# Optimization experiments

Hardware: AMD Instinct MI355X
Metric: run time of the kernel (lower is better)

Reference implementation:

```python
import jax, jax.numpy as jnp
import numpy as np

B, T, C = 256, 2048, 39   # batch, time, nb_filters
NB = 8                     # number of dilation levels (2**0 .. 2**7)
K = 2                      # kernel size
NC = 8                     # num_classes
EPS = 1e-5                 # BatchNorm eps (eval mode)


def _causal_conv(x, w, b, d):
    """x: [B,C,T], w: [Cout,Cin,K], left-pad (K-1)*d for causality."""
    k = w.shape[-1]
    y = jax.lax.conv_general_dilated(
        x, w, window_strides=(1,), padding=[((k - 1) * d, 0)],
        rhs_dilation=(d,), dimension_numbers=('NCH', 'OIH', 'NCH'))
    return y + b[None, :, None]


def _bn(x, g, be, m, v):
    # eval-mode BatchNorm1d with running stats
    return g[None, :, None] * (x - m[None, :, None]) * jax.lax.rsqrt(v + EPS)[None, :, None] + be[None, :, None]


def _block(x, w, b, g, be, m, v, d):
    # Temporal_Aware_Block, eval mode (dropout = identity).
    # w: [2,C,C,K], b/g/be/m/v: [2,C]
    y = jax.nn.relu(_bn(_causal_conv(x, w[0], b[0], d), g[0], be[0], m[0], v[0]))
    y = jax.nn.relu(_bn(_causal_conv(y, w[1], b[1], d), g[1], be[1], m[1], v[1]))
    # causal conv preserves length, so the 1x1 residual conv branch is never taken
    return x * jax.nn.sigmoid(y)


def setup_inputs() -> dict:
    key = jax.random.key(0)
    ks = jax.random.split(key, 24)
    f = lambda k, s: jax.random.normal(k, s, dtype=jnp.float32) * 0.1
    return {
        'inputs': jax.random.normal(ks[0], (B, T, C), dtype=jnp.float32),
        'conv1x1_w': f(ks[1], (C, C, 1)),
        'conv1x1_b': f(ks[2], (C,)),
        'fw_conv_w': f(ks[3], (NB, 2, C, C, K)),
        'fw_conv_b': f(ks[4], (NB, 2, C)),
        'fw_gamma': 1.0 + f(ks[5], (NB, 2, C)),
        'fw_beta': f(ks[6], (NB, 2, C)),
        'fw_mean': f(ks[7], (NB, 2, C)),
        'fw_var': jax.random.uniform(ks[8], (NB, 2, C), dtype=jnp.float32, minval=0.5, maxval=1.5),
        'bw_conv_w': f(ks[9], (NB, 2, C, C, K)),
        'bw_conv_b': f(ks[10], (NB, 2, C)),
        'bw_gamma': 1.0 + f(ks[11], (NB, 2, C)),
        'bw_beta': f(ks[12], (NB, 2, C)),
        'bw_mean': f(ks[13], (NB, 2, C)),
        'bw_var': jax.random.uniform(ks[14], (NB, 2, C), dtype=jnp.float32, minval=0.5, maxval=1.5),
        'wl_kernel': f(ks[15], (NB, 1)),
        'cls_w': f(ks[16], (NC, C)),
        'cls_b': f(ks[17], (NC,)),
    }


def reference(inputs, conv1x1_w, conv1x1_b,
              fw_conv_w, fw_conv_b, fw_gamma, fw_beta, fw_mean, fw_var,
              bw_conv_w, bw_conv_b, bw_gamma, bw_beta, bw_mean, bw_var,
              wl_kernel, cls_w, cls_b):
    x = jnp.transpose(inputs, (0, 2, 1))           # [B,C,T]
    fwd = _causal_conv(x, conv1x1_w, conv1x1_b, 1)
    bwd = _causal_conv(x[:, :, ::-1], conv1x1_w, conv1x1_b, 1)
    skips = []
    for i in range(NB):
        d = 2 ** i
        fwd = _block(fwd, fw_conv_w[i], fw_conv_b[i], fw_gamma[i], fw_beta[i], fw_mean[i], fw_var[i], d)
        bwd = _block(bwd, bw_conv_w[i], bw_conv_b[i], bw_gamma[i], bw_beta[i], bw_mean[i], bw_var[i], d)
        skips.append(jnp.mean(fwd + bwd, axis=-1))  # [B,C]
    g = jnp.stack(skips, axis=-1)                   # [B,C,NB]
    x2 = jnp.einsum('bcn,no->bc', g, wl_kernel)     # WeightLayer matmul + squeeze
    logits = x2 @ cls_w.T + cls_b                   # [B,NC]
    return jax.nn.log_softmax(logits, axis=1)
```

## Files before the change

### kernel.cpp

```cpp
#include <hip/hip_runtime.h>
#include <math.h>

#define BATCH 256
#define TT    2048
#define CC    39
#define CP    40
#define NBLK  8
#define KK    2
#define NCLS  8
#define BN_EPS 1e-5f

typedef __attribute__((ext_vector_type(8))) short short8;
typedef __attribute__((ext_vector_type(4))) float floatx4;

__device__ __forceinline__ unsigned short f2b(float f) {
    union { float f; unsigned u; } v; v.f = f;
    unsigned r = v.u + 0x7FFF + ((v.u >> 16) & 1);
    return (unsigned short)(r >> 16);
}
__device__ __forceinline__ unsigned cvtpk(float lo, float hi) {
    unsigned r;
    asm("v_cvt_pk_bf16_f32 %0, %1, %2" : "=v"(r) : "v"(lo), "v"(hi));
    return r;
}
__device__ __forceinline__ float blo(unsigned u) {
    union { unsigned v; float f; } k; k.v = u << 16; return k.f;
}
__device__ __forceinline__ float bhi(unsigned u) {
    union { unsigned v; float f; } k; k.v = u & 0xffff0000u; return k.f;
}

#define WFB_PER   (2*3*3*512)
#define WFB_TOTAL (2*NBLK*WFB_PER)
#define BFB_TOTAL (2*NBLK*2*48)
#define WFF_TOTAL (3*2*512)
#define BFF_TOTAL 48

__global__ void fold_kernel(const float* __restrict__ fw_w, const float* __restrict__ fw_b,
                            const float* __restrict__ fw_g, const float* __restrict__ fw_be,
                            const float* __restrict__ fw_m, const float* __restrict__ fw_v,
                            const float* __restrict__ bw_w, const float* __restrict__ bw_b,
                            const float* __restrict__ bw_g, const float* __restrict__ bw_be,
                            const float* __restrict__ bw_m, const float* __restrict__ bw_v,
                            const float* __restrict__ c1w, const float* __restrict__ c1b,
                            unsigned short* __restrict__ wfb, float* __restrict__ bfb,
                            unsigned short* __restrict__ wff, float* __restrict__ bff) {
    int idx = blockIdx.x * blockDim.x + threadIdx.x;
    if (idx < WFB_TOTAL) {
        int i = idx;
        int reg = i & 7;   i >>= 3;
        int lane = i & 63; i >>= 6;
        int sl = i % 3;    i /= 3;
        int ct = i % 3;    i /= 3;
        int layer = i & 1; i >>= 1;
        int blk = i & 7;   i >>= 3;
        int dir = i;
        int co = ct * 16 + (lane & 15);
        int kin = ((lane >> 4) << 3) + reg;
        int p = kin >> 4;
        int ci = sl * 16 + (kin & 15);
        float val = 0.f;
        if (co < CC && ci < CC) {
            const float* w = dir ? bw_w : fw_w;
            const float* g = dir ? bw_g : fw_g;
            const float* v = dir ? bw_v : fw_v;
            int il = blk * 2 + layer;
            float sc = g[il * CC + co] * rsqrtf(v[il * CC + co] + BN_EPS);
            val = w[((size_t)(il * CC + co) * CC + ci) * KK + p] * sc;
        }
        wfb[idx] = f2b(val);
        return;
    }
    idx -= WFB_TOTAL;
    if (idx < BFB_TOTAL) {
        int co = idx % 48;
        int i = idx / 48;
        int layer = i & 1; i >>= 1;
        int blk = i & 7;   i >>= 3;
        int dir = i;
        float val = 0.f;
        if (co < CC) {
            const float* b  = dir ? bw_b  : fw_b;
            const float* g  = dir ? bw_g  : fw_g;
            const float* be = dir ? bw_be : fw_be;
            const float* m  = dir ? bw_m  : fw_m;
            const float* v  = dir ? bw_v  : fw_v;
            int r = (blk * 2 + layer) * CC + co;
            float sc = g[r] * rsqrtf(v[r] + BN_EPS);
            val = (b[r] - m[r]) * sc + be[r];
        }
        bfb[idx] = val;
        return;
    }
    idx -= BFB_TOTAL;
    if (idx < WFF_TOTAL) {
        int i = idx;
        int reg = i & 7;   i >>= 3;
        int lane = i & 63; i >>= 6;
        int sl = i & 1;    i >>= 1;
        int ct = i;
        int co = ct * 16 + (lane & 15);
        int ci = sl * 32 + ((lane >> 4) << 3) + reg;
        float val = (co < CC && ci < CC) ? c1w[co * CC + ci] : 0.f;
        wff[idx] = f2b(val);
        return;
    }
    idx -= WFF_TOTAL;
    if (idx < BFF_TOTAL) {
        bff[idx] = (idx < CC) ? c1b[idx] : 0.f;
    }
}

__global__ __launch_bounds__(256) void front_mfma(const float* __restrict__ in,
                                                  const unsigned short* __restrict__ wf,
                                                  const float* __restrict__ bias,
                                                  unsigned short* __restrict__ out) {
    __shared__ unsigned short xt[256 * CP + 32];
    const int dir = blockIdx.z, b = blockIdx.y, t0 = blockIdx.x * 256;
    const int tid = threadIdx.x, lane = tid & 63, wave = tid >> 6;
    const int c = lane & 15, g = lane >> 4;
    const int stmin = dir ? (TT - t0 - 256) : t0;
    const float* src = in + ((size_t)b * TT + stmin) * CC;

    unsigned* xd = (unsigned*)xt;
    for (int e = tid; e < 256 * 20; e += 256) {
        int row = e / 20, cp = e - row * 20;
        int c0 = cp * 2;
        float f0 = src[(size_t)row * CC + c0];
        float f1 = (c0 + 1 < CC) ? src[(size_t)row * CC + c0 + 1] : 0.f;
        xd[row * 20 + cp] = cvtpk(f0, f1);
    }
    if (tid < 16) ((unsigned*)(xt + 256 * CP))[tid] = 0;
    __syncthreads();

    short8 Wf[3][2];
#pragma unroll
    for (int ct = 0; ct < 3; ++ct)
#pragma unroll
        for (int sl = 0; sl < 2; ++sl)
            Wf[ct][sl] = *(const short8*)(wf + (((ct * 2 + sl) * 64 + lane) << 3));
    float bs[3][4];
#pragma unroll
    for (int ct = 0; ct < 3; ++ct)
#pragma unroll
        for (int j = 0; j < 4; ++j) bs[ct][j] = bias[ct * 16 + g * 4 + j];

    for (int mt = wave; mt < 16; mt += 4) {
        int row = (mt << 4) + c;
        const unsigned short* bp = xt + row * CP;
        floatx4 acc[3];
#pragma unroll
        for (int ct = 0; ct < 3; ++ct)
            acc[ct] = floatx4{bs[ct][0], bs[ct][1], bs[ct][2], bs[ct][3]};
#pragma unroll
        for (int sl = 0; sl < 2; ++sl) {
            short8 B = *(const short8*)(bp + sl * 32 + g * 8);
#pragma unroll
            for (int ct = 0; ct < 3; ++ct)
                acc[ct] = __builtin_amdgcn_mfma_f32_16x16x32_bf16(Wf[ct][sl], B, acc[ct], 0, 0, 0);
        }
        int t = dir ? (t0 + 255 - row) : (t0 + row);
        unsigned short* op = out + ((size_t)(dir * BATCH + b) * TT + t) * CP;
#pragma unroll
        for (int ct = 0; ct < 3; ++ct) {
            if (ct == 2 && g >= 2) continue;
            uint2 v;
            v.x = cvtpk(acc[ct][0], acc[ct][1]);
            v.y = cvtpk(acc[ct][2], acc[ct][3]);
            *(uint2*)(op + ct * 16 + g * 4) = v;
        }
    }
}

__global__ __launch_bounds__(256) void block_mfma(const unsigned short* __restrict__ xg,
                                                  unsigned short* __restrict__ yg,
                                                  const unsigned short* __restrict__ wf_all,
                                                  const float* __restrict__ bf_all,
                                                  float* __restrict__ skipPart,
                                                  int d, int blk, int Tt, int writeOut) {
    extern __shared__ char ldsraw[];
    const int dir = blockIdx.z, b = blockIdx.y, tile = blockIdx.x;
    const int t0 = tile * Tt;
    const int tid = threadIdx.x, lane = tid & 63, wave = tid >> 6;
    const int c = lane & 15, g = lane >> 4;
    const int tapoff = (g >> 1) ? d : 0;
    const int koff8 = (g & 1) << 3;
    const int rows_x = Tt + 2 * d;
    const int M1 = (Tt + d + 15) >> 4;
    const int rows_y1 = M1 << 4;
    const int rows_real = Tt + d;

    unsigned short* xt = (unsigned short*)ldsraw;
    unsigned short* y1 = xt + rows_x * CP + 32;
    float* stash = (float*)(y1 + rows_y1 * CP + 32);

    const size_t cbase = (size_t)(dir * BATCH + b) * TT * CP;
    const unsigned short* wf = wf_all + (size_t)(dir * NBLK + blk) * WFB_PER;
    const float* bf = bf_all + (size_t)(dir * NBLK + blk) * 96;

    {
        const uint4* gsrc = (const uint4*)(xg + cbase);
        uint4* ldst = (uint4*)xt;
        int base_t = t0 - 2 * d;
        int nch = rows_x * 5;
        for (int ch = tid; ch < nch; ch += 256) {
            int row = ch / 5;
            int t = base_t + row;
            uint4 v;
            if (t < 0) { v.x = v.y = v.z = v.w = 0u; }
            else       { v = gsrc[(size_t)t * 5 + (ch - row * 5)]; }
            ldst[ch] = v;
        }
        if (tid < 16) ((unsigned*)(xt + (size_t)rows_x * CP))[tid] = 0;
        else if (tid < 32) ((unsigned*)(y1 + (size_t)rows_y1 * CP))[tid - 16] = 0;
    }
    __syncthreads();

    short8 Wf[3][3];
#pragma unroll
    for (int ct = 0; ct < 3; ++ct)
#pragma unroll
        for (int sl = 0; sl < 3; ++sl)
            Wf[ct][sl] = *(const short8*)(wf + ((((0 * 3 + ct) * 3 + sl) * 64 + lane) << 3));
    float bs[3][4];
#pragma unroll
    for (int ct = 0; ct < 3; ++ct)
#pragma unroll
        for (int j = 0; j < 4; ++j) bs[ct][j] = bf[ct * 16 + g * 4 + j];

    for (int mt = wave; mt < M1; mt += 4) {
        int j0 = mt << 4;
        int brow = j0 + c + tapoff;
        const unsigned short* bp = xt + brow * CP + koff8;
        floatx4 acc[3];
#pragma unroll
        for (int ct = 0; ct < 3; ++ct)
            acc[ct] = floatx4{bs[ct][0], bs[ct][1], bs[ct][2], bs[ct][3]};
#pragma unroll
        for (int sl = 0; sl < 3; ++sl) {
            short8 B = *(const short8*)(bp + sl * 16);
#pragma unroll
            for (int ct = 0; ct < 3; ++ct)
                acc[ct] = __builtin_amdgcn_mfma_f32_16x16x32_bf16(Wf[ct][sl], B, acc[ct], 0, 0, 0);
        }
        int r = j0 + c;
        bool dead = (t0 - d + r < 0) || (r >= rows_real);
        unsigned short* yp = y1 + r * CP;
#pragma unroll
        for (int ct = 0; ct < 3; ++ct) {
            if (ct == 2 && g >= 2) continue;
            uint2 v;
            v.x = cvtpk(fmaxf(acc[ct][0], 0.f), fmaxf(acc[ct][1], 0.f));
            v.y = cvtpk(fmaxf(acc[ct][2], 0.f), fmaxf(acc[ct][3], 0.f));
            if (dead) { v.x = 0u; v.y = 0u; }
            *(uint2*)(yp + ct * 16 + g * 4) = v;
        }
    }
    __syncthreads();

#pragma unroll
    for (int ct = 0; ct < 3; ++ct)
#pragma unroll
        for (int sl = 0; sl < 3; ++sl)
            Wf[ct][sl] = *(const short8*)(wf + ((((1 * 3 + ct) * 3 + sl) * 64 + lane) << 3));
#pragma unroll
    for (int ct = 0; ct < 3; ++ct)
#pragma unroll
        for (int j = 0; j < 4; ++j) bs[ct][j] = bf[48 + ct * 16 + g * 4 + j];

    float sums[3][4];
#pragma unroll
    for (int ct = 0; ct < 3; ++ct)
#pragma unroll
        for (int j = 0; j < 4; ++j) sums[ct][j] = 0.f;

    const int M2w = Tt >> 6;
    for (int mi = 0; mi < M2w; ++mi) {
        int j0 = (wave * M2w + mi) << 4;
        int brow = j0 + c + tapoff;
        const unsigned short* bp = y1 + brow * CP + koff8;
        floatx4 acc[3];
#pragma unroll
        for (int ct = 0; ct < 3; ++ct)
            acc[ct] = floatx4{bs[ct][0], bs[ct][1], bs[ct][2], bs[ct][3]};
#pragma unroll
        for (int sl = 0; sl < 3; ++sl) {
            short8 B = *(const short8*)(bp + sl * 16);
#pragma unroll
            for (int ct = 0; ct < 3; ++ct)
                acc[ct] = __builtin_amdgcn_mfma_f32_16x16x32_bf16(Wf[ct][sl], B, acc[ct], 0, 0, 0);
        }
        int r = j0 + c;
        const unsigned short* xrow = xt + (r + 2 * d) * CP;
        unsigned short* orow = yg + cbase + (size_t)(t0 + r) * CP;
#pragma unroll
        for (int ct = 0; ct < 3; ++ct) {
            uint2 xv = *(const uint2*)(xrow + ct * 16 + g * 4);
            float g0 = blo(xv.x) * __builtin_amdgcn_rcpf(1.f + __expf(-acc[ct][0]));
            float g1 = bhi(xv.x) * __builtin_amdgcn_rcpf(1.f + __expf(-acc[ct][1]));
            float g2 = blo(xv.y) * __builtin_amdgcn_rcpf(1.f + __expf(-acc[ct][2]));
            float g3 = bhi(xv.y) * __builtin_amdgcn_rcpf(1.f + __expf(-acc[ct][3]));
            sums[ct][0] += g0; sums[ct][1] += g1;
            sums[ct][2] += g2; sums[ct][3] += g3;
            if (writeOut && !(ct == 2 && g >= 2)) {
                uint2 v;
                v.x = cvtpk(g0, g1);
                v.y = cvtpk(g2, g3);
                *(uint2*)(orow + ct * 16 + g * 4) = v;
            }
        }
    }
#pragma unroll
    for (int ct = 0; ct < 3; ++ct)
#pragma unroll
        for (int j = 0; j < 4; ++j) {
            float v = sums[ct][j];
            v += __shfl_xor(v, 1, 64);
            v += __shfl_xor(v, 2, 64);
            v += __shfl_xor(v, 4, 64);
            v += __shfl_xor(v, 8, 64);
            sums[ct][j] = v;
        }
    if (c == 0) {
#pragma unroll
        for (int ct = 0; ct < 3; ++ct)
#pragma unroll
            for (int j = 0; j < 4; ++j)
                stash[wave * 48 + ct * 16 + g * 4 + j] = sums[ct][j];
    }
    __syncthreads();
    if (tid < CC) {
        float s = stash[tid] + stash[48 + tid] + stash[96 + tid] + stash[144 + tid];
        skipPart[(((size_t)(blk * 2 + dir) * BATCH + b) * CC + tid) * 16 + tile] = s;
    }
}

__global__ __launch_bounds__(64) void tail_kernel(const float* __restrict__ skipPart,
                                                  const float* __restrict__ wl,
                                                  const float* __restrict__ cw,
                                                  const float* __restrict__ cb,
                                                  float* __restrict__ out) {
    __shared__ float xs[CC];
    int b = blockIdx.x;
    int cth = threadIdx.x;
    if (cth < CC) {
        float x2 = 0.f;
        for (int i = 0; i < NBLK; ++i) {
            float wli = wl[i] * (1.0f / TT);
            int nt = (i == NBLK - 1) ? 16 : 8;
            for (int dirn = 0; dirn < 2; ++dirn) {
                const float* sp = skipPart + (((size_t)(i * 2 + dirn) * BATCH + b) * CC + cth) * 16;
                float s = 0.f;
                for (int tl = 0; tl < nt; ++tl) s += sp[tl];
                x2 = fmaf(s, wli, x2);
            }
        }
        xs[cth] = x2;
    }
    __syncthreads();
    if (threadIdx.x == 0) {
        float lg[NCLS];
        float mx = -1e30f;
        for (int o = 0; o < NCLS; ++o) {
            float a = cb[o];
#pragma unroll
            for (int cc2 = 0; cc2 < CC; ++cc2) a = fmaf(cw[o * CC + cc2], xs[cc2], a);
            lg[o] = a;
            mx = fmaxf(mx, a);
        }
        float se = 0.f;
        for (int o = 0; o < NCLS; ++o) se += expf(lg[o] - mx);
        float lse = logf(se) + mx;
        for (int o = 0; o < NCLS; ++o) out[b * NCLS + o] = lg[o] - lse;
    }
}

extern "C" void kernel_launch(void* const* d_in, const int* in_sizes, int n_in,
                              void* d_out, int out_size, void* d_ws, size_t ws_size,
                              hipStream_t stream) {
    const float* inputs = (const float*)d_in[0];
    const float* c1w    = (const float*)d_in[1];
    const float* c1b    = (const float*)d_in[2];
    const float* fw_w   = (const float*)d_in[3];
    const float* fw_b   = (const float*)d_in[4];
    const float* fw_g   = (const float*)d_in[5];
    const float* fw_be  = (const float*)d_in[6];
    const float* fw_m   = (const float*)d_in[7];
    const float* fw_v   = (const float*)d_in[8];
    const float* bw_w   = (const float*)d_in[9];
    const float* bw_b   = (const float*)d_in[10];
    const float* bw_g   = (const float*)d_in[11];
    const float* bw_be  = (const float*)d_in[12];
    const float* bw_m   = (const float*)d_in[13];
    const float* bw_v   = (const float*)d_in[14];
    const float* wl     = (const float*)d_in[15];
    const float* clsw   = (const float*)d_in[16];
    const float* clsb   = (const float*)d_in[17];

    const size_t bufsz = (size_t)2 * BATCH * TT * CP;
    unsigned short* buf0 = (unsigned short*)d_ws;
    unsigned short* buf1 = buf0 + bufsz;
    float* skip = (float*)(buf1 + bufsz);
    const size_t skipsz = (size_t)NBLK * 2 * BATCH * CC * 16;
    unsigned short* wfb = (unsigned short*)(skip + skipsz);
    float* bfb = (float*)(wfb + WFB_TOTAL);
    unsigned short* wff = (unsigned short*)(bfb + BFB_TOTAL);
    float* bff = (float*)(wff + WFF_TOTAL);

    {
        int tot = WFB_TOTAL + BFB_TOTAL + WFF_TOTAL + BFF_TOTAL;
        fold_kernel<<<(tot + 255) / 256, 256, 0, stream>>>(
            fw_w, fw_b, fw_g, fw_be, fw_m, fw_v,
            bw_w, bw_b, bw_g, bw_be, bw_m, bw_v, c1w, c1b,
            wfb, bfb, wff, bff);
    }

    front_mfma<<<dim3(TT / 256, BATCH, 2), 256, 0, stream>>>(inputs, wff, bff, buf0);

    unsigned short* cur = buf0;
    unsigned short* nxt = buf1;
    for (int i = 0; i < NBLK; ++i) {
        int d = 1 << i;
        int Tt = (d == 128) ? 128 : 256;
        int ntl = TT / Tt;
        int rows_x = Tt + 2 * d;
        int M1 = (Tt + d + 15) >> 4;
        int rows_y1 = M1 << 4;
        size_t lds = ((size_t)(rows_x * CP + 32) + (size_t)(rows_y1 * CP + 32)) * 2 + 4 * 48 * 4;
        block_mfma<<<dim3(ntl, BATCH, 2), 256, lds, stream>>>(
            cur, nxt, wfb, bfb, skip, d, i, Tt, (i < NBLK - 1) ? 1 : 0);
        unsigned short* tmp = cur; cur = nxt; nxt = tmp;
    }

    tail_kernel<<<BATCH, 64, 0, stream>>>(skip, wl, clsw, clsb, (float*)d_out);
}
```

Measured before the change: 543.3 us.

## Use direct global-to-LDS loads, template block kernel on dilation, repack K-slices

Tile loading into LDS now uses the global_load_lds builtin, with out-of-range rows served from a zeroed pad buffer, so data no longer passes through VGPRs. The block kernel is templated on dilation and tile length, making loop bounds and offsets compile-time constants. The weight layout for the third K-slice is repacked so that both conv taps of channels 32-39 share one MFMA, which removes a wasted padded slice. The y1 LDS row stride changes to 44 to reduce bank conflicts. This adds a memset, an extra workspace region and eight template instantiations, and the repacked weight layout and loader must match exactly for results to stay correct.

```diff
diff --git a/kernel.cpp b/kernel.cpp
--- a/kernel.cpp
+++ b/kernel.cpp
@@ -5,6 +5,7 @@
 #define TT    2048
 #define CC    39
 #define CP    40
+#define Y1ST  44
 #define NBLK  8
 #define KK    2
 #define NCLS  8
@@ -28,6 +29,11 @@
 }
 __device__ __forceinline__ float bhi(unsigned u) {
     union { unsigned v; float f; } k; k.v = u & 0xffff0000u; return k.f;
+}
+__device__ __forceinline__ void gl_lds16(const void* g, void* l) {
+    __builtin_amdgcn_global_load_lds(
+        (const __attribute__((address_space(1))) unsigned int*)g,
+        (__attribute__((address_space(3))) unsigned int*)l, 16, 0, 0);
 }
 
 #define WFB_PER   (2*3*3*512)
@@ -35,6 +41,7 @@
 #define BFB_TOTAL (2*NBLK*2*48)
 #define WFF_TOTAL (3*2*512)
 #define BFF_TOTAL 48
+#define ZPAD_SHORTS (256 * CP)
 
 __global__ void fold_kernel(const float* __restrict__ fw_w, const float* __restrict__ fw_b,
                             const float* __restrict__ fw_g, const float* __restrict__ fw_be,
@@ -55,17 +62,25 @@
         int layer = i & 1; i >>= 1;
         int blk = i & 7;   i >>= 3;
         int dir = i;
+        int g = lane >> 4;
         int co = ct * 16 + (lane & 15);
-        int kin = ((lane >> 4) << 3) + reg;
-        int p = kin >> 4;
-        int ci = sl * 16 + (kin & 15);
+        int p, ci; bool ok = true;
+        if (sl < 2) {
+            int kin = (g << 3) + reg;
+            p = kin >> 4;
+            ci = sl * 16 + (kin & 15);
+        } else {
+            p = g & 1;
+            ci = 32 + reg;
+            ok = (g < 2);
+        }
         float val = 0.f;
-        if (co < CC && ci < CC) {
+        if (ok && co < CC && ci < CC) {
             const float* w = dir ? bw_w : fw_w;
-            const float* g = dir ? bw_g : fw_g;
-            const float* v = dir ? bw_v : fw_v;
+            const float* gam = dir ? bw_g : fw_g;
+            const float* var = dir ? bw_v : fw_v;
             int il = blk * 2 + layer;
-            float sc = g[il * CC + co] * rsqrtf(v[il * CC + co] + BN_EPS);
+            float sc = gam[il * CC + co] * rsqrtf(var[il * CC + co] + BN_EPS);
             val = w[((size_t)(il * CC + co) * CC + ci) * KK + p] * sc;
         }
         wfb[idx] = f2b(val);
@@ -172,49 +187,53 @@
     }
 }
 
+template <int D, int TtC>
 __global__ __launch_bounds__(256) void block_mfma(const unsigned short* __restrict__ xg,
                                                   unsigned short* __restrict__ yg,
                                                   const unsigned short* __restrict__ wf_all,
                                                   const float* __restrict__ bf_all,
                                                   float* __restrict__ skipPart,
-                                                  int d, int blk, int Tt, int writeOut) {
+                                                  const unsigned short* __restrict__ zpad,
+                                                  int blk, int writeOut) {
+    constexpr int ROWS_X   = TtC + 2 * D;
+    constexpr int NCH      = ROWS_X * 5;
+    constexpr int NIT      = (NCH + 255) / 256;
+    constexpr int XT_SHORTS = NIT * 256 * 8;
+    constexpr int M1       = (TtC + D + 15) / 16;
+    constexpr int ROWS_Y1  = M1 * 16;
+    constexpr int ROWS_REAL = TtC + D;
+    constexpr int Y1_SHORTS = ROWS_Y1 * Y1ST + 8;
+    constexpr int M2W      = TtC / 64;
+
     extern __shared__ char ldsraw[];
+    unsigned short* xt = (unsigned short*)ldsraw;
+    unsigned short* y1 = xt + XT_SHORTS;
+    float* stash = (float*)(y1 + Y1_SHORTS);
+
     const int dir = blockIdx.z, b = blockIdx.y, tile = blockIdx.x;
-    const int t0 = tile * Tt;
+    const int t0 = tile * TtC;
     const int tid = threadIdx.x, lane = tid & 63, wave = tid >> 6;
     const int c = lane & 15, g = lane >> 4;
-    const int tapoff = (g >> 1) ? d : 0;
-    const int koff8 = (g & 1) << 3;
-    const int rows_x = Tt + 2 * d;
-    const int M1 = (Tt + d + 15) >> 4;
-    const int rows_y1 = M1 << 4;
-    const int rows_real = Tt + d;
-
-    unsigned short* xt = (unsigned short*)ldsraw;
-    unsigned short* y1 = xt + rows_x * CP + 32;
-    float* stash = (float*)(y1 + rows_y1 * CP + 32);
 
     const size_t cbase = (size_t)(dir * BATCH + b) * TT * CP;
     const unsigned short* wf = wf_all + (size_t)(dir * NBLK + blk) * WFB_PER;
     const float* bf = bf_all + (size_t)(dir * NBLK + blk) * 96;
 
     {
-        const uint4* gsrc = (const uint4*)(xg + cbase);
-        uint4* ldst = (uint4*)xt;
-        int base_t = t0 - 2 * d;
-        int nch = rows_x * 5;
-        for (int ch = tid; ch < nch; ch += 256) {
-            int row = ch / 5;
-            int t = base_t + row;
-            uint4 v;
-            if (t < 0) { v.x = v.y = v.z = v.w = 0u; }
-            else       { v = gsrc[(size_t)t * 5 + (ch - row * 5)]; }
-            ldst[ch] = v;
-        }
-        if (tid < 16) ((unsigned*)(xt + (size_t)rows_x * CP))[tid] = 0;
-        else if (tid < 32) ((unsigned*)(y1 + (size_t)rows_y1 * CP))[tid - 16] = 0;
-    }
-    __syncthreads();
+        const unsigned short* gx = xg + cbase;
+#pragma unroll
+        for (int it = 0; it < NIT; ++it) {
+            int chunk = it * 256 + wave * 64 + lane;
+            unsigned row = (unsigned)chunk / 5u;
+            int sub = chunk - (int)row * 5;
+            int t = t0 - 2 * D + (int)row;
+            const unsigned short* src = (chunk < NCH && t >= 0)
+                ? (gx + (size_t)t * CP + sub * 8)
+                : (zpad + ((row & 255u) * CP + sub * 8));
+            unsigned short* dst = xt + (size_t)(it * 256 + wave * 64) * 8;
+            gl_lds16(src, dst);
+        }
+    }
 
     short8 Wf[3][3];
 #pragma unroll
@@ -228,24 +247,30 @@
 #pragma unroll
         for (int j = 0; j < 4; ++j) bs[ct][j] = bf[ct * 16 + g * 4 + j];
 
+    __syncthreads();
+
+    const int r01off = (g >> 1) * D;
+    const int r2off  = (g & 1) * D;
+    const int koff8  = (g & 1) << 3;
+
     for (int mt = wave; mt < M1; mt += 4) {
         int j0 = mt << 4;
-        int brow = j0 + c + tapoff;
-        const unsigned short* bp = xt + brow * CP + koff8;
+        const unsigned short* bp01 = xt + (j0 + c + r01off) * CP + koff8;
+        const unsigned short* bp2  = xt + (j0 + c + r2off) * CP + 32;
+        short8 B0 = *(const short8*)(bp01);
+        short8 B1 = *(const short8*)(bp01 + 16);
+        short8 B2 = *(const short8*)(bp2);
         floatx4 acc[3];
 #pragma unroll
-        for (int ct = 0; ct < 3; ++ct)
+        for (int ct = 0; ct < 3; ++ct) {
             acc[ct] = floatx4{bs[ct][0], bs[ct][1], bs[ct][2], bs[ct][3]};
-#pragma unroll
-        for (int sl = 0; sl < 3; ++sl) {
-            short8 B = *(const short8*)(bp + sl * 16);
-#pragma unroll
-            for (int ct = 0; ct < 3; ++ct)
-                acc[ct] = __builtin_amdgcn_mfma_f32_16x16x32_bf16(Wf[ct][sl], B, acc[ct], 0, 0, 0);
+            acc[ct] = __builtin_amdgcn_mfma_f32_16x16x32_bf16(Wf[ct][0], B0, acc[ct], 0, 0, 0);
+            acc[ct] = __builtin_amdgcn_mfma_f32_16x16x32_bf16(Wf[ct][1], B1, acc[ct], 0, 0, 0);
+            acc[ct] = __builtin_amdgcn_mfma_f32_16x16x32_bf16(Wf[ct][2], B2, acc[ct], 0, 0, 0);
         }
         int r = j0 + c;
-        bool dead = (t0 - d + r < 0) || (r >= rows_real);
-        unsigned short* yp = y1 + r * CP;
+        bool dead = (t0 - D + r < 0) || (r >= ROWS_REAL);
+        unsigned short* yp = y1 + r * Y1ST;
 #pragma unroll
         for (int ct = 0; ct < 3; ++ct) {
             if (ct == 2 && g >= 2) continue;
@@ -274,24 +299,24 @@
 #pragma unroll
         for (int j = 0; j < 4; ++j) sums[ct][j] = 0.f;
 
-    const int M2w = Tt >> 6;
-    for (int mi = 0; mi < M2w; ++mi) {
-        int j0 = (wave * M2w + mi) << 4;
-        int brow = j0 + c + tapoff;
-        const unsigned short* bp = y1 + brow * CP + koff8;
+#pragma unroll
+    for (int mi = 0; mi < M2W; ++mi) {
+        int j0 = (wave * M2W + mi) << 4;
+        const unsigned short* bp01 = y1 + (j0 + c + r01off) * Y1ST + koff8;
+        const unsigned short* bp2  = y1 + (j0 + c + r2off) * Y1ST + 32;
+        short8 B0 = *(const short8*)(bp01);
+        short8 B1 = *(const short8*)(bp01 + 16);
+        short8 B2 = *(const short8*)(bp2);
         floatx4 acc[3];
 #pragma unroll
-        for (int ct = 0; ct < 3; ++ct)
+        for (int ct = 0; ct < 3; ++ct) {
             acc[ct] = floatx4{bs[ct][0], bs[ct][1], bs[ct][2], bs[ct][3]};
-#pragma unroll
-        for (int sl = 0; sl < 3; ++sl) {
-            short8 B = *(const short8*)(bp + sl * 16);
-#pragma unroll
-            for (int ct = 0; ct < 3; ++ct)
-                acc[ct] = __builtin_amdgcn_mfma_f32_16x16x32_bf16(Wf[ct][sl], B, acc[ct], 0, 0, 0);
+            acc[ct] = __builtin_amdgcn_mfma_f32_16x16x32_bf16(Wf[ct][0], B0, acc[ct], 0, 0, 0);
+            acc[ct] = __builtin_amdgcn_mfma_f32_16x16x32_bf16(Wf[ct][1], B1, acc[ct], 0, 0, 0);
+            acc[ct] = __builtin_amdgcn_mfma_f32_16x16x32_bf16(Wf[ct][2], B2, acc[ct], 0, 0, 0);
         }
         int r = j0 + c;
-        const unsigned short* xrow = xt + (r + 2 * d) * CP;
+        const unsigned short* xrow = xt + (r + 2 * D) * CP;
         unsigned short* orow = yg + cbase + (size_t)(t0 + r) * CP;
 #pragma unroll
         for (int ct = 0; ct < 3; ++ct) {
@@ -333,6 +358,16 @@
         float s = stash[tid] + stash[48 + tid] + stash[96 + tid] + stash[144 + tid];
         skipPart[(((size_t)(blk * 2 + dir) * BATCH + b) * CC + tid) * 16 + tile] = s;
     }
+}
+
+static inline size_t lds_bytes_for(int D, int Tt) {
+    int rows_x = Tt + 2 * D;
+    int nch = rows_x * 5;
+    int nit = (nch + 255) / 256;
+    int xt_shorts = nit * 256 * 8;
+    int m1 = (Tt + D + 15) / 16;
+    int y1_shorts = m1 * 16 * Y1ST + 8;
+    return (size_t)(xt_shorts + y1_shorts) * 2 + 192 * 4;
 }
 
 __global__ __launch_bounds__(64) void tail_kernel(const float* __restrict__ skipPart,
@@ -406,6 +441,9 @@
     float* bfb = (float*)(wfb + WFB_TOTAL);
     unsigned short* wff = (unsigned short*)(bfb + BFB_TOTAL);
     float* bff = (float*)(wff + WFF_TOTAL);
+    unsigned short* zpad = (unsigned short*)(bff + BFF_TOTAL);
+
+    hipMemsetAsync(zpad, 0, ZPAD_SHORTS * sizeof(unsigned short), stream);
 
     {
         int tot = WFB_TOTAL + BFB_TOTAL + WFF_TOTAL + BFF_TOTAL;
@@ -419,18 +457,24 @@
 
     unsigned short* cur = buf0;
     unsigned short* nxt = buf1;
+#define LAUNCH_BLOCK(DD, TTC)                                                        \
+    block_mfma<DD, TTC><<<dim3(TT / TTC, BATCH, 2), 256, lds_bytes_for(DD, TTC),     \
+                          stream>>>(cur, nxt, wfb, bfb, skip, zpad, i,               \
+                                    (i < NBLK - 1) ? 1 : 0)
     for (int i = 0; i < NBLK; ++i) {
-        int d = 1 << i;
-        int Tt = (d == 128) ? 128 : 256;
-        int ntl = TT / Tt;
-        int rows_x = Tt + 2 * d;
-        int M1 = (Tt + d + 15) >> 4;
-        int rows_y1 = M1 << 4;
-        size_t lds = ((size_t)(rows_x * CP + 32) + (size_t)(rows_y1 * CP + 32)) * 2 + 4 * 48 * 4;
-        block_mfma<<<dim3(ntl, BATCH, 2), 256, lds, stream>>>(
-            cur, nxt, wfb, bfb, skip, d, i, Tt, (i < NBLK - 1) ? 1 : 0);
+        switch (i) {
+            case 0: LAUNCH_BLOCK(1, 256); break;
+            case 1: LAUNCH_BLOCK(2, 256); break;
+            case 2: LAUNCH_BLOCK(4, 256); break;
+            case 3: LAUNCH_BLOCK(8, 256); break;
+            case 4: LAUNCH_BLOCK(16, 256); break;
+            case 5: LAUNCH_BLOCK(32, 256); break;
+            case 6: LAUNCH_BLOCK(64, 256); break;
+            case 7: LAUNCH_BLOCK(128, 128); break;
+        }
         unsigned short* tmp = cur; cur = nxt; nxt = tmp;
     }
+#undef LAUNCH_BLOCK
 
     tail_kernel<<<BATCH, 64, 0, stream>>>(skip, wl, clsw, clsb, (float*)d_out);
 }
```

New measurement: 553.6 us. About the same (+1.9%).
